# Kernel tuning notes

Measured on AMD Instinct MI355X. Metric: run time of the kernel, lower is better.

Reference implementation:

```python
import jax, jax.numpy as jnp
import numpy as np
from jax import lax

T, B, HW, HID, NA = 128, 64, 52, 512, 15  # rollout len, num_envs, image size, lstm hidden, n_actions


def setup_inputs() -> dict:
    key = jax.random.key(0)
    ks = jax.random.split(key, 20)
    BT = T * B
    x = jax.random.uniform(ks[0], (BT, HW, HW, 3), dtype=jnp.float32) * 255.0
    done = jax.random.randint(ks[1], (BT,), 0, 2).astype(jnp.float32)
    h0 = jax.random.normal(ks[2], (B, HID), dtype=jnp.float32) * 0.1
    c0 = jax.random.normal(ks[3], (B, HID), dtype=jnp.float32) * 0.1
    action = jax.random.randint(ks[4], (BT,), 0, NA, dtype=jnp.int32)
    n = lambda k, s, sc: jax.random.normal(k, s, dtype=jnp.float32) * sc
    return {
        "x": x, "done": done, "h0": h0, "c0": c0, "action": action,
        "conv_w1": n(ks[5], (32, 3, 8, 8), 0.05), "conv_b1": jnp.zeros((32,), jnp.float32),
        "conv_w2": n(ks[6], (64, 32, 4, 4), 0.05), "conv_b2": jnp.zeros((64,), jnp.float32),
        "conv_w3": n(ks[7], (64, 64, 3, 3), 0.05), "conv_b3": jnp.zeros((64,), jnp.float32),
        "fc_w": n(ks[8], (576, HID), 0.05), "fc_b": jnp.zeros((HID,), jnp.float32),
        "w_ih": n(ks[9], (4 * HID, HID), 0.04), "w_hh": n(ks[10], (4 * HID, HID), 0.04),
        "b_lstm": jnp.zeros((4 * HID,), jnp.float32),
        "actor_w": n(ks[11], (HID, NA), 0.01), "actor_b": jnp.zeros((NA,), jnp.float32),
        "critic_w": n(ks[12], (HID, 1), 0.05), "critic_b": jnp.zeros((1,), jnp.float32),
    }


def _conv(x, w, b, stride):
    y = lax.conv_general_dilated(x, w, (stride, stride), "VALID",
                                 dimension_numbers=("NCHW", "OIHW", "NCHW"))
    return y + b[None, :, None, None]


def _forward(x, done, h0, c0, conv_w1, conv_b1, conv_w2, conv_b2, conv_w3, conv_b3,
             fc_w, fc_b, w_ih, w_hh, b_lstm, actor_w, actor_b, critic_w, critic_b, action):
    # CNN encoder (input arrives NHWC like the torch caller, permute to NCHW)
    z = jnp.transpose(x, (0, 3, 1, 2)) / 255.0
    z = jax.nn.relu(_conv(z, conv_w1, conv_b1, 4))   # [BT,32,12,12]
    z = jax.nn.relu(_conv(z, conv_w2, conv_b2, 2))   # [BT,64,5,5]
    z = jax.nn.relu(_conv(z, conv_w3, conv_b3, 1))   # [BT,64,3,3]
    z = z.reshape(z.shape[0], -1)                    # [BT,576]
    hidden = jax.nn.relu(z @ fc_w + fc_b)            # [BT,512]

    seq = hidden.reshape(T, B, HID)
    dseq = done.reshape(T, B)

    def step(carry, inp):
        h, c = carry
        xt, dt = inp
        m = (1.0 - dt)[:, None]                       # done-mask resets state
        h, c = h * m, c * m
        gates = xt @ w_ih.T + h @ w_hh.T + b_lstm     # [B,4H], gate order i,f,g,o
        i, f, g, o = jnp.split(gates, 4, axis=-1)
        i, f, o = jax.nn.sigmoid(i), jax.nn.sigmoid(f), jax.nn.sigmoid(o)
        c = f * c + i * jnp.tanh(g)
        h = o * jnp.tanh(c)
        return (h, c), h

    (hT, cT), hs = lax.scan(step, (h0, c0), (seq, dseq))
    feats = hs.reshape(T * B, HID)

    logits = feats @ actor_w + actor_b               # [BT,NA]
    logp = jax.nn.log_softmax(logits)
    lp_a = jnp.take_along_axis(logp, action[:, None], axis=1)[:, 0]
    entropy = -jnp.sum(jnp.exp(logp) * logp, axis=-1)
    value = feats @ critic_w + critic_b              # [BT,1]
    return lp_a, entropy, value, hT, cT


def reference(x, done, h0, c0, conv_w1, conv_b1, conv_w2, conv_b2, conv_w3, conv_b3,
              fc_w, fc_b, w_ih, w_hh, b_lstm, actor_w, actor_b, critic_w, critic_b, action):
    return _forward(x, done, h0, c0, conv_w1, conv_b1, conv_w2, conv_b2, conv_w3, conv_b3,
                    fc_w, fc_b, w_ih, w_hh, b_lstm, actor_w, actor_b, critic_w, critic_b, action)
```

## Files before the change

kernel.cpp:

```cpp
#include <hip/hip_runtime.h>
#include <hip/hip_bf16.h>
#include <math.h>

typedef unsigned short u16;
typedef __attribute__((ext_vector_type(8))) short bf16x8;
typedef __attribute__((ext_vector_type(4))) float f32x4;

__device__ inline u16 f2b(float f) {
  __hip_bfloat16 h = __float2bfloat16(f);
  return *(u16*)&h;
}

__global__ void __launch_bounds__(256) prep_k(
    const float* __restrict__ w1, const float* __restrict__ w2,
    const float* __restrict__ w3, const float* __restrict__ fcw,
    const float* __restrict__ whh, const float* __restrict__ done,
    const float* __restrict__ h0, const float* __restrict__ c0,
    float* __restrict__ w1t, u16* __restrict__ w2bh, u16* __restrict__ w3bh,
    u16* __restrict__ fcwT, float* __restrict__ whhT,
    float* __restrict__ hT0, float* __restrict__ cbuf) {
  int i = blockIdx.x * 256 + threadIdx.x;
  if (i < 6144) {
    int o = i & 31, idx = i >> 5;
    int ch = idx % 3, kyx = idx / 3;
    int ky = kyx >> 3, kx = kyx & 7;
    w1t[i] = w1[((o * 3 + ch) * 8 + ky) * 8 + kx];
    return;
  }
  i -= 6144;
  if (i < 32768) {
    int c = i >> 9, k = i & 511;
    int ci = k & 31, kyx = k >> 5;
    int ky = kyx >> 2, kx = kyx & 3;
    w2bh[i] = f2b(w2[c * 512 + ci * 16 + ky * 4 + kx]);
    return;
  }
  i -= 32768;
  if (i < 36864) {
    int c = i / 576, k = i - c * 576;
    int ci = k & 63, kyx = k >> 6;
    int ky = kyx / 3, kx = kyx - ky * 3;
    w3bh[i] = f2b(w3[((c * 64 + ci) * 3 + ky) * 3 + kx]);
    return;
  }
  i -= 36864;
  if (i < 294912) {
    int o = i / 576, r = i - o * 576;
    int c = r & 63, yx = r >> 6;
    fcwT[i] = f2b(fcw[(c * 9 + yx) * 512 + o]);
    return;
  }
  i -= 294912;
  if (i < 1048576) {
    int j = i & 2047, k = i >> 11;
    whhT[i] = whh[j * 512 + k];
    return;
  }
  i -= 1048576;
  if (i < 32768) {
    int b = i & 63;
    int k = i >> 6;
    hT0[i] = h0[b * 512 + k] * (1.0f - done[b]);
    return;
  }
  i -= 32768;
  if (i < 32768) {
    int b = i >> 9;
    cbuf[i] = c0[i] * (1.0f - done[b]);
  }
}

__global__ void __launch_bounds__(256) conv1_k(
    const float* __restrict__ x, const float* __restrict__ w1t,
    const float* __restrict__ b1, u16* __restrict__ a1h) {
  __shared__ float img[8112];
  __shared__ float wt[6144];
  const int n = blockIdx.x;
  const int tid = threadIdx.x;
  const float* xp = x + (long)n * 8112;
  for (int i = tid; i < 8112; i += 256) img[i] = xp[i] * (1.0f / 255.0f);
  for (int i = tid; i < 6144; i += 256) wt[i] = w1t[i];
  __syncthreads();
  const int cq = tid & 7;
  const int pg = tid >> 3;
  const bool extra = pg < 16;
  float4 bias = *(const float4*)&b1[cq * 4];
  float4 acc[5];
  int base[5];
#pragma unroll
  for (int i = 0; i < 5; ++i) {
    acc[i] = make_float4(0.f, 0.f, 0.f, 0.f);
    int p = pg + 32 * i;
    if (p > 143) p = 143;
    int py = p / 12, px = p - py * 12;
    base[i] = py * 624 + px * 12;
  }
  for (int ky = 0; ky < 8; ++ky) {
    const int ib = ky * 156;
    const int wb = ky * 24 * 32;
#pragma unroll
    for (int kxc = 0; kxc < 24; ++kxc) {
      float4 w = *(const float4*)&wt[wb + kxc * 32 + cq * 4];
#pragma unroll
      for (int i = 0; i < 4; ++i) {
        float v = img[base[i] + ib + kxc];
        acc[i].x += v * w.x; acc[i].y += v * w.y;
        acc[i].z += v * w.z; acc[i].w += v * w.w;
      }
      if (extra) {
        float v = img[base[4] + ib + kxc];
        acc[4].x += v * w.x; acc[4].y += v * w.y;
        acc[4].z += v * w.z; acc[4].w += v * w.w;
      }
    }
  }
#pragma unroll
  for (int i = 0; i < 5; ++i) {
    int p = pg + 32 * i;
    if (p < 144) {
      ushort4 o;
      o.x = f2b(fmaxf(acc[i].x + bias.x, 0.f));
      o.y = f2b(fmaxf(acc[i].y + bias.y, 0.f));
      o.z = f2b(fmaxf(acc[i].z + bias.z, 0.f));
      o.w = f2b(fmaxf(acc[i].w + bias.w, 0.f));
      *(ushort4*)&a1h[(long)n * 4608 + p * 32 + cq * 4] = o;
    }
  }
}

__global__ void __launch_bounds__(256) conv2m_k(
    const u16* __restrict__ a1h, const u16* __restrict__ w2bh,
    const float* __restrict__ b2, u16* __restrict__ a2h) {
  __shared__ u16 As[256 * 40];
  __shared__ u16 Bs[64 * 40];
  const int tid = threadIdx.x;
  const long bm = (long)blockIdx.x * 256;
  const int w = tid >> 6;
  const int lane = tid & 63;
  const int lr = lane & 15;
  const int lk = lane >> 4;
  const int wm = w * 64;
  const int r = (int)bm + tid;
  const int n = r / 25;
  const int p = r - n * 25;
  const int py = p / 5;
  const int px = p - py * 5;
  const int pbase = n * 4608 + (py * 24 + px * 2) * 32;
  f32x4 zero = {0.f, 0.f, 0.f, 0.f};
  f32x4 acc[4][4];
#pragma unroll
  for (int mi = 0; mi < 4; ++mi)
#pragma unroll
    for (int ni = 0; ni < 4; ++ni) acc[mi][ni] = zero;

  for (int ks = 0; ks < 16; ++ks) {
    const int koff = ((ks >> 2) * 12 + (ks & 3)) * 32;
#pragma unroll
    for (int q = 0; q < 4; ++q)
      *(uint4*)&As[tid * 40 + q * 8] = *(const uint4*)&a1h[pbase + koff + q * 8];
    {
      const int c = tid >> 2, q = tid & 3;
      *(uint4*)&Bs[c * 40 + q * 8] = *(const uint4*)&w2bh[c * 512 + ks * 32 + q * 8];
    }
    __syncthreads();
    bf16x8 af[4], bfr[4];
#pragma unroll
    for (int mi = 0; mi < 4; ++mi)
      af[mi] = *(const bf16x8*)&As[(wm + mi * 16 + lr) * 40 + lk * 8];
#pragma unroll
    for (int ni = 0; ni < 4; ++ni)
      bfr[ni] = *(const bf16x8*)&Bs[(ni * 16 + lr) * 40 + lk * 8];
#pragma unroll
    for (int mi = 0; mi < 4; ++mi)
#pragma unroll
      for (int ni = 0; ni < 4; ++ni)
        acc[mi][ni] = __builtin_amdgcn_mfma_f32_16x16x32_bf16(
            af[mi], bfr[ni], acc[mi][ni], 0, 0, 0);
    __syncthreads();
  }
#pragma unroll
  for (int ni = 0; ni < 4; ++ni) {
    float bv = b2[ni * 16 + lr];
#pragma unroll
    for (int mi = 0; mi < 4; ++mi) {
#pragma unroll
      for (int j = 0; j < 4; ++j) {
        long rg = bm + wm + mi * 16 + lk * 4 + j;
        float v = fmaxf(acc[mi][ni][j] + bv, 0.f);
        a2h[rg * 64 + ni * 16 + lr] = f2b(v);
      }
    }
  }
}

__global__ void __launch_bounds__(256) conv3m_k(
    const u16* __restrict__ a2h, const u16* __restrict__ w3bh,
    const float* __restrict__ b3, u16* __restrict__ a3h) {
  __shared__ u16 As[256 * 40];
  __shared__ u16 Bs[64 * 40];
  const int tid = threadIdx.x;
  const long bm = (long)blockIdx.x * 256;
  const int w = tid >> 6;
  const int lane = tid & 63;
  const int lr = lane & 15;
  const int lk = lane >> 4;
  const int wm = w * 64;
  const int r = (int)bm + tid;
  const int n = r / 9;
  const int p = r - n * 9;
  const int py = p / 3;
  const int px = p - py * 3;
  const int pbase = n * 1600 + (py * 5 + px) * 64;
  f32x4 zero = {0.f, 0.f, 0.f, 0.f};
  f32x4 acc[4][4];
#pragma unroll
  for (int mi = 0; mi < 4; ++mi)
#pragma unroll
    for (int ni = 0; ni < 4; ++ni) acc[mi][ni] = zero;

  for (int ks2 = 0; ks2 < 18; ++ks2) {
    const int tap = ks2 >> 1;
    const int ky = tap / 3, kx = tap - ky * 3;
    const int koff = (ky * 5 + kx) * 64 + (ks2 & 1) * 32;
#pragma unroll
    for (int q = 0; q < 4; ++q)
      *(uint4*)&As[tid * 40 + q * 8] = *(const uint4*)&a2h[pbase + koff + q * 8];
    {
      const int c = tid >> 2, q = tid & 3;
      *(uint4*)&Bs[c * 40 + q * 8] = *(const uint4*)&w3bh[c * 576 + ks2 * 32 + q * 8];
    }
    __syncthreads();
    bf16x8 af[4], bfr[4];
#pragma unroll
    for (int mi = 0; mi < 4; ++mi)
      af[mi] = *(const bf16x8*)&As[(wm + mi * 16 + lr) * 40 + lk * 8];
#pragma unroll
    for (int ni = 0; ni < 4; ++ni)
      bfr[ni] = *(const bf16x8*)&Bs[(ni * 16 + lr) * 40 + lk * 8];
#pragma unroll
    for (int mi = 0; mi < 4; ++mi)
#pragma unroll
      for (int ni = 0; ni < 4; ++ni)
        acc[mi][ni] = __builtin_amdgcn_mfma_f32_16x16x32_bf16(
            af[mi], bfr[ni], acc[mi][ni], 0, 0, 0);
    __syncthreads();
  }
#pragma unroll
  for (int ni = 0; ni < 4; ++ni) {
    float bv = b3[ni * 16 + lr];
#pragma unroll
    for (int mi = 0; mi < 4; ++mi) {
#pragma unroll
      for (int j = 0; j < 4; ++j) {
        long rg = bm + wm + mi * 16 + lk * 4 + j;
        float v = fmaxf(acc[mi][ni][j] + bv, 0.f);
        a3h[rg * 64 + ni * 16 + lr] = f2b(v);
      }
    }
  }
}

__global__ void __launch_bounds__(256) cast_k(
    const float4* __restrict__ wihv, ushort4* __restrict__ wihh) {
  int i = blockIdx.x * 256 + threadIdx.x;
  if (i < 262144) {
    float4 v = wihv[i];
    ushort4 o;
    o.x = f2b(v.x); o.y = f2b(v.y); o.z = f2b(v.z); o.w = f2b(v.w);
    wihh[i] = o;
  }
}

__global__ void __launch_bounds__(256) mgemm_k(
    const u16* __restrict__ A, const u16* __restrict__ B,
    const float* __restrict__ bias, float* __restrict__ Cf,
    u16* __restrict__ Ch, const int K, const int N,
    const int RELU, const int OUTBF16) {
  __shared__ u16 As[128 * 40];
  __shared__ u16 Bs[128 * 40];
  const int tid = threadIdx.x;
  const long bm = (long)blockIdx.x * 128;
  const long bn = (long)blockIdx.y * 128;
  const int w = tid >> 6;
  const int lane = tid & 63;
  const int lr = lane & 15;
  const int lk = lane >> 4;
  const int wm = (w >> 1) * 64, wn = (w & 1) * 64;
  f32x4 zero = {0.f, 0.f, 0.f, 0.f};
  f32x4 acc[4][4];
#pragma unroll
  for (int mi = 0; mi < 4; ++mi)
#pragma unroll
    for (int ni = 0; ni < 4; ++ni) acc[mi][ni] = zero;

  for (int k0 = 0; k0 < K; k0 += 32) {
#pragma unroll
    for (int q = 0; q < 2; ++q) {
      int idx = tid * 2 + q;
      int row = idx >> 2, kq = (idx & 3) * 8;
      *(uint4*)&As[row * 40 + kq] = *(const uint4*)&A[(bm + row) * K + k0 + kq];
      *(uint4*)&Bs[row * 40 + kq] = *(const uint4*)&B[(bn + row) * K + k0 + kq];
    }
    __syncthreads();
    bf16x8 af[4], bfr[4];
#pragma unroll
    for (int mi = 0; mi < 4; ++mi)
      af[mi] = *(const bf16x8*)&As[(wm + mi * 16 + lr) * 40 + lk * 8];
#pragma unroll
    for (int ni = 0; ni < 4; ++ni)
      bfr[ni] = *(const bf16x8*)&Bs[(wn + ni * 16 + lr) * 40 + lk * 8];
#pragma unroll
    for (int mi = 0; mi < 4; ++mi)
#pragma unroll
      for (int ni = 0; ni < 4; ++ni)
        acc[mi][ni] = __builtin_amdgcn_mfma_f32_16x16x32_bf16(
            af[mi], bfr[ni], acc[mi][ni], 0, 0, 0);
    __syncthreads();
  }
#pragma unroll
  for (int ni = 0; ni < 4; ++ni) {
    float bv = bias[bn + wn + ni * 16 + lr];
#pragma unroll
    for (int mi = 0; mi < 4; ++mi) {
#pragma unroll
      for (int j = 0; j < 4; ++j) {
        long rg = bm + wm + mi * 16 + lk * 4 + j;
        long cg = bn + wn + ni * 16 + lr;
        float v = acc[mi][ni][j] + bv;
        if (RELU) v = fmaxf(v, 0.f);
        if (OUTBF16) Ch[rg * N + cg] = f2b(v);
        else Cf[rg * N + cg] = v;
      }
    }
  }
}

__global__ void __launch_bounds__(256) lstm_step_k(
    const float* __restrict__ gx, const float* __restrict__ whhT,
    const float* __restrict__ done, float* __restrict__ hT2,
    float* __restrict__ cbuf, float* __restrict__ hseq,
    float* __restrict__ outh, float* __restrict__ outc, const int t) {
  __shared__ float red[256][37];
  const int tid = threadIdx.x;
  const int bid = blockIdx.x;
  const int uslice = (bid & 7) * 4 + (bid >> 6);
  const int bg = (bid >> 3) & 7;
  const int uu = tid & 15;
  const int kc = tid >> 4;
  const int u = uslice * 16 + uu;
  const int b0 = bg * 8;
  const int fbl = tid >> 4;

  const float* hTp = hT2 + (t & 1) * 32768;
  float a0[8] = {0.f}, a1_[8] = {0.f}, a2_[8] = {0.f}, a3_[8] = {0.f};
  const int kbeg = kc * 32;
#pragma unroll 4
  for (int kk = 0; kk < 32; ++kk) {
    int k = kbeg + kk;
    const float* wr = whhT + k * 2048;
    float w0 = wr[u];
    float w1 = wr[u + 512];
    float w2 = wr[u + 1024];
    float w3 = wr[u + 1536];
    float hv[8];
    *(float4*)&hv[0] = *(const float4*)&hTp[k * 64 + b0];
    *(float4*)&hv[4] = *(const float4*)&hTp[k * 64 + b0 + 4];
#pragma unroll
    for (int j = 0; j < 8; ++j) {
      a0[j] += w0 * hv[j]; a1_[j] += w1 * hv[j];
      a2_[j] += w2 * hv[j]; a3_[j] += w3 * hv[j];
    }
  }
#pragma unroll
  for (int j = 0; j < 8; ++j) {
    red[tid][j] = a0[j];       red[tid][8 + j] = a1_[j];
    red[tid][16 + j] = a2_[j]; red[tid][24 + j] = a3_[j];
  }
  __syncthreads();
  if (fbl < 8) {
    float s0 = 0.f, s1 = 0.f, s2 = 0.f, s3 = 0.f;
#pragma unroll
    for (int q = 0; q < 16; ++q) {
      const float* rp = red[q * 16 + uu];
      s0 += rp[fbl]; s1 += rp[8 + fbl]; s2 += rp[16 + fbl]; s3 += rp[24 + fbl];
    }
    const int b = b0 + fbl;
    const int ug = uslice * 16 + uu;
    const int row = t * 64 + b;
    const float* gxr = gx + (long)row * 2048;
    float pi = s0 + gxr[ug];
    float pf = s1 + gxr[512 + ug];
    float pg_ = s2 + gxr[1024 + ug];
    float po = s3 + gxr[1536 + ug];
    float ig = 1.f / (1.f + expf(-pi));
    float fg = 1.f / (1.f + expf(-pf));
    float og = 1.f / (1.f + expf(-po));
    float gg = tanhf(pg_);
    float cn = fg * cbuf[b * 512 + ug] + ig * gg;
    float hn = og * tanhf(cn);
    hseq[(long)row * 512 + ug] = hn;
    if (t == 127) {
      outh[b * 512 + ug] = hn;
      outc[b * 512 + ug] = cn;
    } else {
      float mn = 1.f - done[(t + 1) * 64 + b];
      cbuf[b * 512 + ug] = cn * mn;
      hT2[((t + 1) & 1) * 32768 + ug * 64 + b] = hn * mn;
    }
  }
}

__global__ void __launch_bounds__(256) heads_k(
    const float* __restrict__ hseq, const float* __restrict__ aw,
    const float* __restrict__ ab, const float* __restrict__ cw,
    const float* __restrict__ cb, const int* __restrict__ action,
    float* __restrict__ out) {
  const int lane = threadIdx.x & 63;
  const int wid = threadIdx.x >> 6;
  const int row = blockIdx.x * 4 + wid;
  const int j = lane & 15;
  const int kc = lane >> 4;
  const float* f = hseq + (long)row * 512;
  float acc = 0.f;
  if (j < 15) {
    for (int k = kc * 128; k < kc * 128 + 128; ++k) acc += f[k] * aw[k * 15 + j];
  } else {
    for (int k = kc * 128; k < kc * 128 + 128; ++k) acc += f[k] * cw[k];
  }
  acc += __shfl_xor(acc, 16);
  acc += __shfl_xor(acc, 32);
  float logit = (j < 15) ? acc + ab[j] : -1e30f;
  float m = logit;
#pragma unroll
  for (int off = 1; off < 16; off <<= 1) m = fmaxf(m, __shfl_xor(m, off));
  float p = (j < 15) ? expf(logit - m) : 0.f;
  float S = p;
#pragma unroll
  for (int off = 1; off < 16; off <<= 1) S += __shfl_xor(S, off);
  float logS = logf(S);
  float lp = logit - m - logS;
  float e = (j < 15) ? p * lp : 0.f;
  float es = e;
#pragma unroll
  for (int off = 1; off < 16; off <<= 1) es += __shfl_xor(es, off);
  float ent = -es / S;
  int a = action[row];
  float lpa = __shfl(lp, (lane & 48) | a);
  float val = __shfl(acc, (lane & 48) | 15) + cb[0];
  if (lane == 0) {
    out[row] = lpa;
    out[8192 + row] = ent;
    out[16384 + row] = val;
  }
}

extern "C" void kernel_launch(void* const* d_in, const int* in_sizes, int n_in,
                              void* d_out, int out_size, void* d_ws, size_t ws_size,
                              hipStream_t stream) {
  const float* x    = (const float*)d_in[0];
  const float* done = (const float*)d_in[1];
  const float* h0   = (const float*)d_in[2];
  const float* c0   = (const float*)d_in[3];
  const int*   act  = (const int*)d_in[4];
  const float* w1   = (const float*)d_in[5];
  const float* b1   = (const float*)d_in[6];
  const float* w2   = (const float*)d_in[7];
  const float* b2   = (const float*)d_in[8];
  const float* w3   = (const float*)d_in[9];
  const float* b3   = (const float*)d_in[10];
  const float* fcw  = (const float*)d_in[11];
  const float* fcb  = (const float*)d_in[12];
  const float* wih  = (const float*)d_in[13];
  const float* whh  = (const float*)d_in[14];
  const float* blst = (const float*)d_in[15];
  const float* aw   = (const float*)d_in[16];
  const float* ab   = (const float*)d_in[17];
  const float* cw   = (const float*)d_in[18];
  const float* cb   = (const float*)d_in[19];
  float* ws  = (float*)d_ws;
  float* out = (float*)d_out;

  u16*  a1h   = (u16*)ws;
  u16*  wihh  = (u16*)(ws + 4718592);
  float* hseq = ws + 8912896;
  u16*  a2h   = (u16*)(ws + 37748736);
  u16*  a3h   = (u16*)(ws + 44302336);
  u16*  hidh  = (u16*)(ws + 46661632);
  float* gxb  = ws + 50855936;
  float* w1t  = ws + 67633152;
  u16*  w2bh  = (u16*)(ws + 67639296);
  u16*  w3bh  = (u16*)(ws + 67672064);
  u16*  fcwT  = (u16*)(ws + 67708928);
  float* whhT = ws + 68003840;
  float* hT2  = ws + 69052416;
  float* cbuf = ws + 69117952;

  hipLaunchKernelGGL(prep_k, dim3(5800), dim3(256), 0, stream,
                     w1, w2, w3, fcw, whh, done, h0, c0,
                     w1t, w2bh, w3bh, fcwT, whhT, hT2, cbuf);
  hipLaunchKernelGGL(conv1_k, dim3(8192), dim3(256), 0, stream, x, w1t, b1, a1h);
  hipLaunchKernelGGL(conv2m_k, dim3(800), dim3(256), 0, stream, a1h, w2bh, b2, a2h);
  hipLaunchKernelGGL(conv3m_k, dim3(288), dim3(256), 0, stream, a2h, w3bh, b3, a3h);
  hipLaunchKernelGGL(cast_k, dim3(1024), dim3(256), 0, stream,
                     (const float4*)wih, (ushort4*)wihh);
  hipLaunchKernelGGL(mgemm_k, dim3(64, 4), dim3(256), 0, stream,
                     a3h, fcwT, fcb, (float*)nullptr, hidh, 576, 512, 1, 1);
  hipLaunchKernelGGL(mgemm_k, dim3(64, 16), dim3(256), 0, stream,
                     hidh, wihh, blst, gxb, (u16*)nullptr, 512, 2048, 0, 0);
  for (int t = 0; t < 128; ++t) {
    hipLaunchKernelGGL(lstm_step_k, dim3(256), dim3(256), 0, stream,
                       gxb, whhT, done, hT2, cbuf, hseq,
                       out + 24576, out + 57344, t);
  }
  hipLaunchKernelGGL(heads_k, dim3(2048), dim3(256), 0, stream,
                     hseq, aw, ab, cw, cb, act, out);
}
```

Before: 1.517 ms.

## Rewrite conv1 as implicit-GEMM on bf16 MFMA with scale folded into weights

Replaces the FP32 scalar direct-convolution conv1 kernel with an implicit-GEMM kernel. Each thread loads one output pixel's 8x24 input patch row by row, converts it to bf16 in shared memory, and the block accumulates with 16x16x32 bf16 MFMA instructions. The 1/255 input scaling moves into the pre-cast bf16 conv1 weights, and K is padded from 24 to 32 per kernel row. This removes the FP32 FMA-bound inner loop at the cost of bf16 rounding of the raw 0-255 pixel inputs and of uncoalesced strided patch loads from global memory.

```diff
diff --git a/kernel.cpp b/kernel.cpp
--- a/kernel.cpp
+++ b/kernel.cpp
@@ -16,18 +16,22 @@
     const float* __restrict__ w3, const float* __restrict__ fcw,
     const float* __restrict__ whh, const float* __restrict__ done,
     const float* __restrict__ h0, const float* __restrict__ c0,
-    float* __restrict__ w1t, u16* __restrict__ w2bh, u16* __restrict__ w3bh,
+    u16* __restrict__ w1bh, u16* __restrict__ w2bh, u16* __restrict__ w3bh,
     u16* __restrict__ fcwT, float* __restrict__ whhT,
     float* __restrict__ hT0, float* __restrict__ cbuf) {
   int i = blockIdx.x * 256 + threadIdx.x;
-  if (i < 6144) {
-    int o = i & 31, idx = i >> 5;
-    int ch = idx % 3, kyx = idx / 3;
-    int ky = kyx >> 3, kx = kyx & 7;
-    w1t[i] = w1[((o * 3 + ch) * 8 + ky) * 8 + kx];
+  if (i < 8192) {
+    int c = i >> 8, k = i & 255;
+    int ky = k >> 5, rem = k & 31;
+    float v = 0.f;
+    if (rem < 24) {
+      int kx = rem / 3, ch = rem - kx * 3;
+      v = w1[((c * 3 + ch) * 8 + ky) * 8 + kx] * (1.0f / 255.0f);
+    }
+    w1bh[i] = f2b(v);
     return;
   }
-  i -= 6144;
+  i -= 8192;
   if (i < 32768) {
     int c = i >> 9, k = i & 511;
     int ci = k & 31, kyx = k >> 5;
@@ -70,60 +74,78 @@
   }
 }
 
-__global__ void __launch_bounds__(256) conv1_k(
-    const float* __restrict__ x, const float* __restrict__ w1t,
+__global__ void __launch_bounds__(256) conv1m_k(
+    const float* __restrict__ x, const u16* __restrict__ w1bh,
     const float* __restrict__ b1, u16* __restrict__ a1h) {
-  __shared__ float img[8112];
-  __shared__ float wt[6144];
-  const int n = blockIdx.x;
+  __shared__ u16 As[256 * 40];
+  __shared__ u16 Bs[32 * 40];
   const int tid = threadIdx.x;
-  const float* xp = x + (long)n * 8112;
-  for (int i = tid; i < 8112; i += 256) img[i] = xp[i] * (1.0f / 255.0f);
-  for (int i = tid; i < 6144; i += 256) wt[i] = w1t[i];
-  __syncthreads();
-  const int cq = tid & 7;
-  const int pg = tid >> 3;
-  const bool extra = pg < 16;
-  float4 bias = *(const float4*)&b1[cq * 4];
-  float4 acc[5];
-  int base[5];
-#pragma unroll
-  for (int i = 0; i < 5; ++i) {
-    acc[i] = make_float4(0.f, 0.f, 0.f, 0.f);
-    int p = pg + 32 * i;
-    if (p > 143) p = 143;
-    int py = p / 12, px = p - py * 12;
-    base[i] = py * 624 + px * 12;
-  }
+  const long bm = (long)blockIdx.x * 256;
+  const int w = tid >> 6;
+  const int lane = tid & 63;
+  const int lr = lane & 15;
+  const int lk = lane >> 4;
+  const int wm = w * 64;
+  const int r = (int)bm + tid;
+  const int n = r / 144;
+  const int p = r - n * 144;
+  const int py = p / 12;
+  const int px = p - py * 12;
+  const long gbase = (long)n * 8112 + py * 624 + px * 12;
+  f32x4 zero = {0.f, 0.f, 0.f, 0.f};
+  f32x4 acc[4][2];
+#pragma unroll
+  for (int mi = 0; mi < 4; ++mi)
+#pragma unroll
+    for (int ni = 0; ni < 2; ++ni) acc[mi][ni] = zero;
+
+  const ushort4 z4 = {0, 0, 0, 0};
   for (int ky = 0; ky < 8; ++ky) {
-    const int ib = ky * 156;
-    const int wb = ky * 24 * 32;
-#pragma unroll
-    for (int kxc = 0; kxc < 24; ++kxc) {
-      float4 w = *(const float4*)&wt[wb + kxc * 32 + cq * 4];
-#pragma unroll
-      for (int i = 0; i < 4; ++i) {
-        float v = img[base[i] + ib + kxc];
-        acc[i].x += v * w.x; acc[i].y += v * w.y;
-        acc[i].z += v * w.z; acc[i].w += v * w.w;
+    const float* src = x + gbase + ky * 156;
+    float4 v[6];
+#pragma unroll
+    for (int q = 0; q < 6; ++q) v[q] = *(const float4*)&src[q * 4];
+    u16* dst = &As[tid * 40];
+#pragma unroll
+    for (int q = 0; q < 6; ++q) {
+      ushort4 o;
+      o.x = f2b(v[q].x); o.y = f2b(v[q].y);
+      o.z = f2b(v[q].z); o.w = f2b(v[q].w);
+      *(ushort4*)&dst[q * 4] = o;
+    }
+    *(ushort4*)&dst[24] = z4;
+    *(ushort4*)&dst[28] = z4;
+    if (tid < 128) {
+      const int c = tid >> 2, q = tid & 3;
+      *(uint4*)&Bs[c * 40 + q * 8] = *(const uint4*)&w1bh[c * 256 + ky * 32 + q * 8];
+    }
+    __syncthreads();
+    bf16x8 af[4], bfr[2];
+#pragma unroll
+    for (int mi = 0; mi < 4; ++mi)
+      af[mi] = *(const bf16x8*)&As[(wm + mi * 16 + lr) * 40 + lk * 8];
+#pragma unroll
+    for (int ni = 0; ni < 2; ++ni)
+      bfr[ni] = *(const bf16x8*)&Bs[(ni * 16 + lr) * 40 + lk * 8];
+#pragma unroll
+    for (int mi = 0; mi < 4; ++mi)
+#pragma unroll
+      for (int ni = 0; ni < 2; ++ni)
+        acc[mi][ni] = __builtin_amdgcn_mfma_f32_16x16x32_bf16(
+            af[mi], bfr[ni], acc[mi][ni], 0, 0, 0);
+    __syncthreads();
+  }
+#pragma unroll
+  for (int ni = 0; ni < 2; ++ni) {
+    float bv = b1[ni * 16 + lr];
+#pragma unroll
+    for (int mi = 0; mi < 4; ++mi) {
+#pragma unroll
+      for (int j = 0; j < 4; ++j) {
+        long rg = bm + wm + mi * 16 + lk * 4 + j;
+        float v = fmaxf(acc[mi][ni][j] + bv, 0.f);
+        a1h[rg * 32 + ni * 16 + lr] = f2b(v);
       }
-      if (extra) {
-        float v = img[base[4] + ib + kxc];
-        acc[4].x += v * w.x; acc[4].y += v * w.y;
-        acc[4].z += v * w.z; acc[4].w += v * w.w;
-      }
-    }
-  }
-#pragma unroll
-  for (int i = 0; i < 5; ++i) {
-    int p = pg + 32 * i;
-    if (p < 144) {
-      ushort4 o;
-      o.x = f2b(fmaxf(acc[i].x + bias.x, 0.f));
-      o.y = f2b(fmaxf(acc[i].y + bias.y, 0.f));
-      o.z = f2b(fmaxf(acc[i].z + bias.z, 0.f));
-      o.w = f2b(fmaxf(acc[i].w + bias.w, 0.f));
-      *(ushort4*)&a1h[(long)n * 4608 + p * 32 + cq * 4] = o;
     }
   }
 }
@@ -487,7 +509,7 @@
   u16*  a3h   = (u16*)(ws + 44302336);
   u16*  hidh  = (u16*)(ws + 46661632);
   float* gxb  = ws + 50855936;
-  float* w1t  = ws + 67633152;
+  u16*  w1bh  = (u16*)(ws + 67633152);
   u16*  w2bh  = (u16*)(ws + 67639296);
   u16*  w3bh  = (u16*)(ws + 67672064);
   u16*  fcwT  = (u16*)(ws + 67708928);
@@ -495,10 +517,10 @@
   float* hT2  = ws + 69052416;
   float* cbuf = ws + 69117952;
 
-  hipLaunchKernelGGL(prep_k, dim3(5800), dim3(256), 0, stream,
+  hipLaunchKernelGGL(prep_k, dim3(5808), dim3(256), 0, stream,
                      w1, w2, w3, fcw, whh, done, h0, c0,
-                     w1t, w2bh, w3bh, fcwT, whhT, hT2, cbuf);
-  hipLaunchKernelGGL(conv1_k, dim3(8192), dim3(256), 0, stream, x, w1t, b1, a1h);
+                     w1bh, w2bh, w3bh, fcwT, whhT, hT2, cbuf);
+  hipLaunchKernelGGL(conv1m_k, dim3(4608), dim3(256), 0, stream, x, w1bh, b1, a1h);
   hipLaunchKernelGGL(conv2m_k, dim3(800), dim3(256), 0, stream, a1h, w2bh, b2, a2h);
   hipLaunchKernelGGL(conv3m_k, dim3(288), dim3(256), 0, stream, a2h, w3bh, b3, a3h);
   hipLaunchKernelGGL(cast_k, dim3(1024), dim3(256), 0, stream,
```

Result: faster. 1.281 ms (-15.6%).
